# Kernel optimization log

Hardware: AMD Instinct MI355X
Metric: run time of the kernel (lower is better)

The kernel has to match this reference:

```python
import jax, jax.numpy as jnp
import numpy as np
from math import sqrt

B, LQ, LKV = 4, 1024, 1024
QD = KD = VD = 1024
MODEL_DIM = 1024
H = 16
HD = MODEL_DIM // H  # per-head model_dim = 64


def setup_inputs() -> dict:
    key = jax.random.key(0)
    ks = jax.random.split(key, 10)
    s = 0.02
    return {
        "queries": jax.random.normal(ks[0], (B, LQ, QD), jnp.float32),
        "context": jax.random.normal(ks[1], (B, LKV, KD), jnp.float32),
        # stacked per-head linear weights (torch Linear: y = x @ W.T + b); store as [H, in, out]
        "Wq": jax.random.normal(ks[2], (H, QD, HD), jnp.float32) * s,
        "bq": jax.random.normal(ks[3], (H, HD), jnp.float32) * s,
        "Wk": jax.random.normal(ks[4], (KD, HD * 1 * H), jnp.float32).reshape(H, KD, HD) * s,
        "bk": jax.random.normal(ks[5], (H, HD), jnp.float32) * s,
        "Wv": jax.random.normal(ks[6], (H, VD, HD), jnp.float32) * s,
        "bv": jax.random.normal(ks[7], (H, HD), jnp.float32) * s,
        "Wo": jax.random.normal(ks[8], (H * HD, MODEL_DIM), jnp.float32) * s,
        "bo": jax.random.normal(ks[9], (MODEL_DIM,), jnp.float32) * s,
    }


def reference(queries, context, Wq, bq, Wk, bk, Wv, bv, Wo, bo):
    # queries: [B,Lq,Dq]; context: [B,Lkv,Dk]
    # Per-head projections, batched over heads (equivalent to the torch per-head loop).
    q = jnp.einsum("bld,hdm->bhlm", queries, Wq) + bq[None, :, None, :]  # [B,H,Lq,hd]
    k = jnp.einsum("bld,hdm->bhlm", context, Wk) + bk[None, :, None, :]  # [B,H,Lkv,hd]
    v = jnp.einsum("bld,hdm->bhlm", context, Wv) + bv[None, :, None, :]  # [B,H,Lkv,hd]

    scale = 1.0 / sqrt(HD)
    scores = jnp.einsum("bhqd,bhkd->bhqk", q, k) * scale  # [B,H,Lq,Lkv]
    att = jax.nn.softmax(scores, axis=-1)
    head_out = jnp.einsum("bhqk,bhkd->bhqd", att, v)  # [B,H,Lq,hd]

    # torch concatenates heads along the last dim in head order 0..H-1
    multi = head_out.transpose(0, 2, 1, 3).reshape(B, LQ, H * HD)
    residual = q.transpose(0, 2, 1, 3).reshape(B, LQ, H * HD)

    out = multi @ Wo + bo  # [B,Lq,model_dim]
    return out, residual
```

## Files before the change

kernel.cpp:

```cpp
#include <hip/hip_runtime.h>
#include <hip/hip_bf16.h>


typedef unsigned short u16;
typedef __attribute__((ext_vector_type(8))) short short8;
typedef __attribute__((ext_vector_type(4))) float f32x4;

__device__ __forceinline__ float bf2f(u16 u) {
    union { unsigned int i; float f; } c;
    c.i = ((unsigned int)u) << 16;
    return c.f;
}

__device__ __forceinline__ u16 f2bf(float f) {
    unsigned int x = __float_as_uint(f);
    unsigned int r = (x + 0x7fffu + ((x >> 16) & 1u)) >> 16;
    return (u16)r;
}

__device__ __forceinline__ void glds16(u16* lds, const u16* g) {
    __builtin_amdgcn_global_load_lds(
        (const __attribute__((address_space(1))) void*)g,
        (__attribute__((address_space(3))) void*)lds, 16, 0, 0);
}

#define FENCE() asm volatile("" ::: "memory")
#define BAR() do { FENCE(); __builtin_amdgcn_s_barrier(); FENCE(); } while (0)
#define WAIT_LGKM0() do { asm volatile("s_waitcnt lgkmcnt(0)" ::: "memory"); \
                          __builtin_amdgcn_sched_barrier(0); } while (0)
#define WAIT_VM6() do { asm volatile("s_waitcnt vmcnt(6)" ::: "memory"); \
                        __builtin_amdgcn_sched_barrier(0); } while (0)
#define WAIT_VM4() do { asm volatile("s_waitcnt vmcnt(4)" ::: "memory"); \
                        __builtin_amdgcn_sched_barrier(0); } while (0)
#define WAIT_VM0() do { asm volatile("s_waitcnt vmcnt(0)" ::: "memory"); \
                        __builtin_amdgcn_sched_barrier(0); } while (0)

__global__ __launch_bounds__(256) void prep(
    const float* __restrict__ q, const float* __restrict__ ctx,
    const float* __restrict__ Wq, const float* __restrict__ Wk,
    const float* __restrict__ Wv, const float* __restrict__ Wo,
    u16* __restrict__ Aq, u16* __restrict__ Ac,
    u16* __restrict__ Wqt, u16* __restrict__ Wkt,
    u16* __restrict__ Wvt, u16* __restrict__ Wot)
{
    __shared__ float ls[64][65];
    const int t = threadIdx.x;
    int bid = blockIdx.x;

    if (bid < 4096) {
        const float* in = (bid < 2048) ? q : ctx;
        u16* out = (bid < 2048) ? Aq : Ac;
        size_t i = ((size_t)(bid & 2047) * 256 + t) * 8;
        float4 v0 = *(const float4*)(in + i);
        float4 v1 = *(const float4*)(in + i + 4);
        short8 p;
        p[0] = (short)f2bf(v0.x); p[1] = (short)f2bf(v0.y);
        p[2] = (short)f2bf(v0.z); p[3] = (short)f2bf(v0.w);
        p[4] = (short)f2bf(v1.x); p[5] = (short)f2bf(v1.y);
        p[6] = (short)f2bf(v1.z); p[7] = (short)f2bf(v1.w);
        *(short8*)(out + i) = p;
        return;
    }
    bid -= 4096;
    const float* in; u16* out; int C; size_t moff; int rt, ct;
    if (bid < 768) {
        const int m = bid >> 8, idx = bid & 255;
        in = (m == 0) ? Wq : (m == 1) ? Wk : Wv;
        out = (m == 0) ? Wqt : (m == 1) ? Wkt : Wvt;
        C = 64; rt = (idx & 15) * 64; ct = 0; moff = (size_t)(idx >> 4) * 65536;
    } else {
        const int idx = bid - 768;
        in = Wo; out = Wot; C = 1024; moff = 0;
        rt = (idx & 15) * 64; ct = (idx >> 4) * 64;
    }
    #pragma unroll
    for (int i = 0; i < 4; ++i) {
        int s = i * 256 + t;
        int row = s >> 4, chunk = s & 15;
        float4 v = *(const float4*)(in + moff + (size_t)(rt + row) * C + ct + chunk * 4);
        ls[row][chunk * 4 + 0] = v.x;
        ls[row][chunk * 4 + 1] = v.y;
        ls[row][chunk * 4 + 2] = v.z;
        ls[row][chunk * 4 + 3] = v.w;
    }
    __syncthreads();
    #pragma unroll
    for (int i = 0; i < 2; ++i) {
        int s = i * 256 + t;
        int n = s >> 3, kc = s & 7;
        short8 p;
        #pragma unroll
        for (int j = 0; j < 8; ++j) p[j] = (short)f2bf(ls[kc * 8 + j][n]);
        *(short8*)(out + moff + (size_t)(ct + n) * 1024 + rt + kc * 8) = p;
    }
}

__global__ __launch_bounds__(512) void gemm_qkv8(
    const u16* __restrict__ Aq, const u16* __restrict__ Ac,
    const u16* __restrict__ Wqt, const u16* __restrict__ Wkt,
    const u16* __restrict__ Wvt,
    const float* __restrict__ bq, const float* __restrict__ bk,
    const float* __restrict__ bv,
    u16* __restrict__ qws, u16* __restrict__ kws, u16* __restrict__ vtws)
{
    __shared__ u16 lds[2][2][256 * 64];

    const int tid = threadIdx.x;
    const int w = tid >> 6, lane = tid & 63;
    const int wr = w >> 2, wc = w & 3;
    const int quad = lane >> 4, c = lane & 15, cx = c & 7;
    const int sr = tid >> 3;
    const int gch = (tid & 7) ^ (sr & 7);

    const int f = blockIdx.x;
    const int xcd = f & 7, r = f >> 3;
    const int z = r >> 3;
    const int mt = xcd * 2 + ((r >> 2) & 1);
    const int nt = r & 3;
    const int m0 = mt * 256, n0 = nt * 256;

    const u16* A = (z == 0) ? Aq : Ac;
    const u16* Wt = (z == 0) ? Wqt : (z == 1) ? Wkt : Wvt;
    const float* bias = (z == 0) ? bq : (z == 1) ? bk : bv;

    const u16* gAt = A + (size_t)(m0 + sr) * 1024 + gch * 8;
    const u16* gBt = Wt + (size_t)(n0 + sr) * 1024 + gch * 8;

    auto stageA = [&](int par, int half, int t) {
        const u16* g = gAt + (size_t)half * 128 * 1024 + t * 64;
        u16* l = &lds[par][0][(half * 128 + w * 8) * 64];
        glds16(l, g);
        glds16(l + 64 * 64, g + (size_t)64 * 1024);
    };
    auto stageB = [&](int par, int half, int t) {
        const u16* g = gBt + (size_t)half * 128 * 1024 + t * 64;
        u16* l = &lds[par][1][(half * 128 + w * 8) * 64];
        glds16(l, g);
        glds16(l + 64 * 64, g + (size_t)64 * 1024);
    };

    f32x4 acc[8][4] = {};
    short8 aq[4][2], bA[2][2], bB[2][2];

    auto ldA = [&](int par, int mh) {
        #pragma unroll
        for (int mf = 0; mf < 4; ++mf)
            #pragma unroll
            for (int ks = 0; ks < 2; ++ks)
                aq[mf][ks] = *(const short8*)&lds[par][0][
                    (wr * 128 + mh * 64 + mf * 16 + c) * 64 + (((ks * 4 + quad) ^ cx) * 8)];
    };
    auto ldB = [&](int par, int nh, short8 (&bq_)[2][2]) {
        #pragma unroll
        for (int nf = 0; nf < 2; ++nf)
            #pragma unroll
            for (int ks = 0; ks < 2; ++ks)
                bq_[nf][ks] = *(const short8*)&lds[par][1][
                    (wc * 64 + nh * 32 + nf * 16 + c) * 64 + (((ks * 4 + quad) ^ cx) * 8)];
    };
    auto mma = [&](int mh, int nh, short8 (&bq_)[2][2]) {
        #pragma unroll
        for (int mf = 0; mf < 4; ++mf)
            #pragma unroll
            for (int nf = 0; nf < 2; ++nf)
                #pragma unroll
                for (int ks = 0; ks < 2; ++ks)
                    acc[mh * 4 + mf][nh * 2 + nf] =
                        __builtin_amdgcn_mfma_f32_16x16x32_bf16(
                            aq[mf][ks], bq_[nf][ks], acc[mh * 4 + mf][nh * 2 + nf], 0, 0, 0);
    };

    stageB(0, 0, 0); stageB(0, 1, 0); stageA(0, 0, 0); stageA(0, 1, 0);
    stageB(1, 0, 1); stageB(1, 1, 1);
    WAIT_VM4(); BAR();

    #pragma unroll 1
    for (int i = 0; i < 8; ++i) {
        const int o = 2 * i + 1, e = 2 * i + 2;

        ldA(0, 0); ldB(0, 0, bA);
        stageA(1, 0, o);
        BAR(); WAIT_LGKM0();
        __builtin_amdgcn_s_setprio(1); mma(0, 0, bA); __builtin_amdgcn_s_setprio(0);
        BAR();
        ldB(0, 1, bB);
        stageA(1, 1, o);
        BAR(); WAIT_LGKM0();
        __builtin_amdgcn_s_setprio(1); mma(0, 1, bB); __builtin_amdgcn_s_setprio(0);
        BAR();
        ldA(0, 1);
        if (i < 7) stageB(0, 0, e);
        BAR(); WAIT_LGKM0();
        __builtin_amdgcn_s_setprio(1); mma(1, 1, bB); __builtin_amdgcn_s_setprio(0);
        BAR();
        if (i < 7) stageB(0, 1, e);
        BAR();
        __builtin_amdgcn_s_setprio(1); mma(1, 0, bA); __builtin_amdgcn_s_setprio(0);
        if (i < 7) { WAIT_VM4(); } else { WAIT_VM0(); }
        BAR();
        ldA(1, 0); ldB(1, 0, bA);
        if (i < 7) stageA(0, 0, e);
        BAR(); WAIT_LGKM0();
        __builtin_amdgcn_s_setprio(1); mma(0, 0, bA); __builtin_amdgcn_s_setprio(0);
        BAR();
        ldB(1, 1, bB);
        if (i < 7) stageA(0, 1, e);
        BAR(); WAIT_LGKM0();
        __builtin_amdgcn_s_setprio(1); mma(0, 1, bB); __builtin_amdgcn_s_setprio(0);
        BAR();
        ldA(1, 1);
        if (i < 7) stageB(1, 0, e + 1);
        BAR(); WAIT_LGKM0();
        __builtin_amdgcn_s_setprio(1); mma(1, 1, bB); __builtin_amdgcn_s_setprio(0);
        BAR();
        if (i < 7) stageB(1, 1, e + 1);
        BAR();
        __builtin_amdgcn_s_setprio(1); mma(1, 0, bA); __builtin_amdgcn_s_setprio(0);
        if (i < 7) WAIT_VM4();
        BAR();
    }

    const int h = nt * 4 + wc;
    const int b = m0 >> 10;
    const int lbase = (m0 & 1023) + wr * 128;

    float bb[4];
    #pragma unroll
    for (int cn = 0; cn < 4; ++cn)
        bb[cn] = bias[h * 64 + (cn >> 1) * 32 + (cn & 1) * 16 + c];

    if (z < 2) {
        u16* dst = (z == 0) ? qws : kws;
        const float scale = (z == 0) ? 0.125f : 1.0f;
        u16* dbase = dst + (size_t)(b * 16 + h) * 1024 * 64;
        #pragma unroll
        for (int mi = 0; mi < 8; ++mi) {
            const int ro = (mi >> 2) * 64 + (mi & 3) * 16;
            const int rowb = lbase + ro + quad * 4;
            #pragma unroll
            for (int rr = 0; rr < 4; ++rr) {
                u16* drow = dbase + (size_t)(rowb + rr) * 64;
                #pragma unroll
                for (int cn = 0; cn < 4; ++cn) {
                    const int hd = (cn >> 1) * 32 + (cn & 1) * 16 + c;
                    drow[hd] = f2bf((acc[mi][cn][rr] + bb[cn]) * scale);
                }
            }
        }
    } else {
        u16* dbase = vtws + (size_t)(b * 16 + h) * 64 * 1024;
        #pragma unroll
        for (int mi = 0; mi < 8; ++mi) {
            const int ro = (mi >> 2) * 64 + (mi & 3) * 16;
            const int l0 = lbase + ro + quad * 4;
            #pragma unroll
            for (int cn = 0; cn < 4; ++cn) {
                const int hd = (cn >> 1) * 32 + (cn & 1) * 16 + c;
                ushort4 pk;
                pk.x = f2bf(acc[mi][cn][0] + bb[cn]);
                pk.y = f2bf(acc[mi][cn][1] + bb[cn]);
                pk.z = f2bf(acc[mi][cn][2] + bb[cn]);
                pk.w = f2bf(acc[mi][cn][3] + bb[cn]);
                *(ushort4*)(dbase + (size_t)hd * 1024 + l0) = pk;
            }
        }
    }
}

__global__ __launch_bounds__(256) void gemm_out(
    const u16* __restrict__ A, const u16* __restrict__ Wot,
    const float* __restrict__ bo, float* __restrict__ out)
{
    __shared__ u16 As[2][128 * 64];
    __shared__ u16 Bs[2][64 * 64];
    const int f = blockIdx.x;
    const int xcd = f & 7, k = f >> 3;
    const int m0 = (xcd * 4 + (k & 3)) * 128;
    const int n0 = (k >> 2) * 64;
    const int t = threadIdx.x;
    const int w = t >> 6, lane = t & 63;
    const int quad = lane >> 4, c = lane & 15;
    const int cx = c & 7;

    const int sr = w * 8 + (lane >> 3);
    const int gch = (lane & 7) ^ ((lane >> 3) & 7);
    const u16* gA = A + (size_t)(m0 + sr) * 1024 + gch * 8;
    const u16* gB = Wot + (size_t)(n0 + sr) * 1024 + gch * 8;

    const int arow = (w >> 1) * 64 + c;
    const int brow = (w & 1) * 32 + c;

    auto stage = [&](int par, int kt) {
        #pragma unroll
        for (int i = 0; i < 4; ++i)
            glds16(As[par] + (i * 32 + w * 8) * 64, gA + (size_t)i * 32 * 1024 + kt);
        #pragma unroll
        for (int i = 0; i < 2; ++i)
            glds16(Bs[par] + (i * 32 + w * 8) * 64, gB + (size_t)i * 32 * 1024 + kt);
    };

    f32x4 acc[4][2] = {};
    stage(0, 0);
    stage(1, 64);
    #pragma unroll 1
    for (int i = 0; i < 16; ++i) {
        const int cur = i & 1;
        if (i < 15) { WAIT_VM6(); } else { WAIT_VM0(); }
        BAR();
        #pragma unroll
        for (int kh = 0; kh < 2; ++kh) {
            const int ch = (kh * 4 + quad);
            short8 af[4], bf[2];
            #pragma unroll
            for (int rs = 0; rs < 4; ++rs)
                af[rs] = *(const short8*)(As[cur] + (arow + rs * 16) * 64 + (ch ^ cx) * 8);
            #pragma unroll
            for (int cs = 0; cs < 2; ++cs)
                bf[cs] = *(const short8*)(Bs[cur] + (brow + cs * 16) * 64 + (ch ^ cx) * 8);
            #pragma unroll
            for (int rs = 0; rs < 4; ++rs)
                #pragma unroll
                for (int cs = 0; cs < 2; ++cs)
                    acc[rs][cs] = __builtin_amdgcn_mfma_f32_16x16x32_bf16(
                        af[rs], bf[cs], acc[rs][cs], 0, 0, 0);
        }
        BAR();
        if (i < 14) stage(cur, (i + 2) * 64);
    }

    const int nb = n0 + (w & 1) * 32;
    float bb[2];
    #pragma unroll
    for (int cs = 0; cs < 2; ++cs) bb[cs] = bo[nb + cs * 16 + c];

    #pragma unroll
    for (int rs = 0; rs < 4; ++rs) {
        #pragma unroll
        for (int r = 0; r < 4; ++r) {
            const int row = m0 + (w >> 1) * 64 + rs * 16 + quad * 4 + r;
            float* orow = out + (size_t)row * 1024 + nb;
            #pragma unroll
            for (int cs = 0; cs < 2; ++cs)
                orow[cs * 16 + c] = acc[rs][cs][r] + bb[cs];
        }
    }
}

__global__ __launch_bounds__(256) void attn_mfma(
    const u16* __restrict__ qws, const u16* __restrict__ kws,
    const u16* __restrict__ vtws, u16* __restrict__ multi,
    float* __restrict__ resid)
{
    __shared__ u16 Ks[2][64 * 64];
    __shared__ u16 Vs[2][64 * 64];
    __shared__ u16 Ps[4][16 * 64];
    const int t = threadIdx.x;
    const int wave = t >> 6, lane = t & 63;
    const int quad = lane >> 4, c = lane & 15;
    const int cx = c & 7;
    const int f = blockIdx.x;
    const int xcd = f & 7, j = f >> 3;
    const int bh = xcd * 8 + (j & 7);
    const int qt = j >> 3;
    const int b = bh >> 4, h = bh & 15;
    const int q0 = qt * 128 + wave * 32;

    const u16* qb = qws + ((size_t)bh * 1024 + q0) * 64;
    const u16* kb = kws + (size_t)bh * 65536;
    const u16* vb = vtws + (size_t)bh * 65536;

    short8 qa[2][2];
    #pragma unroll
    for (int rb = 0; rb < 2; ++rb) {
        qa[rb][0] = *(const short8*)(qb + (size_t)(rb * 16 + c) * 64 + quad * 8);
        qa[rb][1] = *(const short8*)(qb + (size_t)(rb * 16 + c) * 64 + 32 + quad * 8);
    }

    const int srow = wave * 16 + (lane >> 3);
    const int gch = (lane & 7) ^ ((lane >> 3) & 7);
    const u16* gK0 = kb + (size_t)srow * 64 + gch * 8;
    const u16* gK1 = kb + (size_t)(srow + 8) * 64 + gch * 8;
    const u16* gV0 = vb + (size_t)srow * 1024 + gch * 8;
    const u16* gV1 = vb + (size_t)(srow + 8) * 1024 + gch * 8;

    auto stage = [&](int par, int kt) {
        glds16(Ks[par] + (wave * 16) * 64,     gK0 + (size_t)kt * 64);
        glds16(Ks[par] + (wave * 16 + 8) * 64, gK1 + (size_t)kt * 64);
        glds16(Vs[par] + (wave * 16) * 64,     gV0 + kt);
        glds16(Vs[par] + (wave * 16 + 8) * 64, gV1 + kt);
    };

    f32x4 O[2][4] = {};
    float ps[2][4] = {};
    u16* pw = &Ps[wave][0];

    stage(0, 0);
    stage(1, 64);

    #pragma unroll 1
    for (int i = 0; i < 16; ++i) {
        const int cur = i & 1;
        if (i < 15) { WAIT_VM4(); } else { WAIT_VM0(); }
        BAR();

        const u16* Kc = Ks[cur];
        const u16* Vc = Vs[cur];

        short8 kf[4][2], vf[4][2];
        #pragma unroll
        for (int nt = 0; nt < 4; ++nt) {
            const u16* kr = Kc + (nt * 16 + c) * 64;
            kf[nt][0] = *(const short8*)(kr + ((quad ^ cx)) * 8);
            kf[nt][1] = *(const short8*)(kr + (((4 + quad) ^ cx)) * 8);
            const u16* vr = Vc + (nt * 16 + c) * 64;
            vf[nt][0] = *(const short8*)(vr + ((quad ^ cx)) * 8);
            vf[nt][1] = *(const short8*)(vr + (((4 + quad) ^ cx)) * 8);
        }

        #pragma unroll
        for (int rb = 0; rb < 2; ++rb) {
            f32x4 s[4];
            __builtin_amdgcn_s_setprio(1);
            #pragma unroll
            for (int nt = 0; nt < 4; ++nt) {
                f32x4 z = {};
                z = __builtin_amdgcn_mfma_f32_16x16x32_bf16(qa[rb][0], kf[nt][0], z, 0, 0, 0);
                z = __builtin_amdgcn_mfma_f32_16x16x32_bf16(qa[rb][1], kf[nt][1], z, 0, 0, 0);
                s[nt] = z;
            }
            __builtin_amdgcn_s_setprio(0);

            #pragma unroll
            for (int nt = 0; nt < 4; ++nt)
                #pragma unroll
                for (int r = 0; r < 4; ++r) {
                    float p = __expf(s[nt][r]);
                    ps[rb][r] += p;
                    const int prow = quad * 4 + r;
                    pw[prow * 64 + (((nt * 2 + (c >> 3)) ^ (prow & 7)) * 8) + (c & 7)]
                        = (u16)(__float_as_uint(p) >> 16);
                }
            short8 pa0 = *(const short8*)(pw + c * 64 + ((quad ^ cx)) * 8);
            short8 pa1 = *(const short8*)(pw + c * 64 + (((4 + quad) ^ cx)) * 8);

            __builtin_amdgcn_s_setprio(1);
            #pragma unroll
            for (int nt = 0; nt < 4; ++nt) {
                O[rb][nt] = __builtin_amdgcn_mfma_f32_16x16x32_bf16(pa0, vf[nt][0], O[rb][nt], 0, 0, 0);
                O[rb][nt] = __builtin_amdgcn_mfma_f32_16x16x32_bf16(pa1, vf[nt][1], O[rb][nt], 0, 0, 0);
            }
            __builtin_amdgcn_s_setprio(0);
        }

        BAR();
        if (i < 14) stage(cur, (i + 2) * 64);
    }

    #pragma unroll
    for (int rb = 0; rb < 2; ++rb) {
        float inv[4];
        #pragma unroll
        for (int r = 0; r < 4; ++r) {
            float sum = ps[rb][r];
            sum += __shfl_xor(sum, 1);
            sum += __shfl_xor(sum, 2);
            sum += __shfl_xor(sum, 4);
            sum += __shfl_xor(sum, 8);
            inv[r] = 1.0f / sum;
        }
        u16* ob = multi + ((size_t)b * 1024 + q0 + rb * 16 + quad * 4) * 1024 + h * 64 + c;
        #pragma unroll
        for (int r = 0; r < 4; ++r) {
            u16* orow = ob + (size_t)r * 1024;
            orow[0]  = f2bf(O[rb][0][r] * inv[r]);
            orow[16] = f2bf(O[rb][1][r] * inv[r]);
            orow[32] = f2bf(O[rb][2][r] * inv[r]);
            orow[48] = f2bf(O[rb][3][r] * inv[r]);
        }

        float* rr = resid + ((size_t)b * 1024 + q0 + rb * 16 + c) * 1024 + h * 64;
        #pragma unroll
        for (int jj = 0; jj < 8; ++jj) {
            rr[quad * 8 + jj]      = bf2f((u16)qa[rb][0][jj]) * 8.0f;
            rr[32 + quad * 8 + jj] = bf2f((u16)qa[rb][1][jj]) * 8.0f;
        }
    }
}

extern "C" void kernel_launch(void* const* d_in, const int* in_sizes, int n_in,
                              void* d_out, int out_size, void* d_ws, size_t ws_size,
                              hipStream_t stream) {
    const float* queries = (const float*)d_in[0];
    const float* context = (const float*)d_in[1];
    const float* Wq = (const float*)d_in[2];
    const float* bq = (const float*)d_in[3];
    const float* Wk = (const float*)d_in[4];
    const float* bk = (const float*)d_in[5];
    const float* Wv = (const float*)d_in[6];
    const float* bv = (const float*)d_in[7];
    const float* Wo = (const float*)d_in[8];
    const float* bo = (const float*)d_in[9];

    float* out = (float*)d_out;
    float* resid = out + (size_t)4 * 1024 * 1024;

    const size_t M1 = 1024 * 1024;
    u16* Aq   = (u16*)d_ws;
    u16* Ac   = Aq + 4 * M1;
    u16* Wqt  = Ac + 4 * M1;
    u16* Wkt  = Wqt + M1;
    u16* Wvt  = Wkt + M1;
    u16* Wot  = Wvt + M1;
    u16* qws  = Wot + M1;
    u16* kws  = qws + 4 * M1;
    u16* vtws = kws + 4 * M1;
    u16* mws  = vtws + 4 * M1;

    prep<<<5120, 256, 0, stream>>>(queries, context, Wq, Wk, Wv, Wo,
                                   Aq, Ac, Wqt, Wkt, Wvt, Wot);
    gemm_qkv8<<<192, 512, 0, stream>>>(Aq, Ac, Wqt, Wkt, Wvt,
                                       bq, bk, bv, qws, kws, vtws);
    attn_mfma<<<512, 256, 0, stream>>>(qws, kws, vtws, mws, resid);
    gemm_out<<<512, 256, 0, stream>>>(mws, Wot, bo, out);
}
```

Baseline: 190.8 us.

## Replace 8-phase interleaved QKV GEMM schedule with simple double-buffered loop

The QKV projection GEMM drops its hand-interleaved 8-phase schedule, which split tile staging across many barriers and used setprio around MFMA groups. It now uses a plain double-buffered loop: wait for the current tile, run all four MFMA quadrants, then issue the global-to-LDS load for the tile two steps ahead. This cuts barrier count and scheduling complexity, but gives up the fine-grained overlap of LDS reads and global loads with MFMA work and removes the explicit priority hints.

```diff
diff --git a/kernel.cpp b/kernel.cpp
--- a/kernel.cpp
+++ b/kernel.cpp
@@ -26,8 +26,8 @@
 
 #define FENCE() asm volatile("" ::: "memory")
 #define BAR() do { FENCE(); __builtin_amdgcn_s_barrier(); FENCE(); } while (0)
-#define WAIT_LGKM0() do { asm volatile("s_waitcnt lgkmcnt(0)" ::: "memory"); \
-                          __builtin_amdgcn_sched_barrier(0); } while (0)
+#define WAIT_VM8() do { asm volatile("s_waitcnt vmcnt(8)" ::: "memory"); \
+                        __builtin_amdgcn_sched_barrier(0); } while (0)
 #define WAIT_VM6() do { asm volatile("s_waitcnt vmcnt(6)" ::: "memory"); \
                         __builtin_amdgcn_sched_barrier(0); } while (0)
 #define WAIT_VM4() do { asm volatile("s_waitcnt vmcnt(4)" ::: "memory"); \
@@ -95,7 +95,7 @@
     }
 }
 
-__global__ __launch_bounds__(512) void gemm_qkv8(
+__global__ __launch_bounds__(512) void gemm_qkv2(
     const u16* __restrict__ Aq, const u16* __restrict__ Ac,
     const u16* __restrict__ Wqt, const u16* __restrict__ Wkt,
     const u16* __restrict__ Wvt,
@@ -126,17 +126,14 @@
     const u16* gAt = A + (size_t)(m0 + sr) * 1024 + gch * 8;
     const u16* gBt = Wt + (size_t)(n0 + sr) * 1024 + gch * 8;
 
-    auto stageA = [&](int par, int half, int t) {
-        const u16* g = gAt + (size_t)half * 128 * 1024 + t * 64;
-        u16* l = &lds[par][0][(half * 128 + w * 8) * 64];
-        glds16(l, g);
-        glds16(l + 64 * 64, g + (size_t)64 * 1024);
-    };
-    auto stageB = [&](int par, int half, int t) {
-        const u16* g = gBt + (size_t)half * 128 * 1024 + t * 64;
-        u16* l = &lds[par][1][(half * 128 + w * 8) * 64];
-        glds16(l, g);
-        glds16(l + 64 * 64, g + (size_t)64 * 1024);
+    auto stage = [&](int par, int t) {
+        #pragma unroll
+        for (int i = 0; i < 4; ++i) {
+            glds16(&lds[par][0][(i * 64 + w * 8) * 64],
+                   gAt + (size_t)(i * 64) * 1024 + t * 64);
+            glds16(&lds[par][1][(i * 64 + w * 8) * 64],
+                   gBt + (size_t)(i * 64) * 1024 + t * 64);
+        }
     };
 
     f32x4 acc[8][4] = {};
@@ -170,54 +167,23 @@
                             aq[mf][ks], bq_[nf][ks], acc[mh * 4 + mf][nh * 2 + nf], 0, 0, 0);
     };
 
-    stageB(0, 0, 0); stageB(0, 1, 0); stageA(0, 0, 0); stageA(0, 1, 0);
-    stageB(1, 0, 1); stageB(1, 1, 1);
-    WAIT_VM4(); BAR();
-
+    stage(0, 0);
+    stage(1, 1);
     #pragma unroll 1
-    for (int i = 0; i < 8; ++i) {
-        const int o = 2 * i + 1, e = 2 * i + 2;
-
-        ldA(0, 0); ldB(0, 0, bA);
-        stageA(1, 0, o);
-        BAR(); WAIT_LGKM0();
-        __builtin_amdgcn_s_setprio(1); mma(0, 0, bA); __builtin_amdgcn_s_setprio(0);
-        BAR();
-        ldB(0, 1, bB);
-        stageA(1, 1, o);
-        BAR(); WAIT_LGKM0();
-        __builtin_amdgcn_s_setprio(1); mma(0, 1, bB); __builtin_amdgcn_s_setprio(0);
-        BAR();
-        ldA(0, 1);
-        if (i < 7) stageB(0, 0, e);
-        BAR(); WAIT_LGKM0();
-        __builtin_amdgcn_s_setprio(1); mma(1, 1, bB); __builtin_amdgcn_s_setprio(0);
-        BAR();
-        if (i < 7) stageB(0, 1, e);
-        BAR();
-        __builtin_amdgcn_s_setprio(1); mma(1, 0, bA); __builtin_amdgcn_s_setprio(0);
-        if (i < 7) { WAIT_VM4(); } else { WAIT_VM0(); }
-        BAR();
-        ldA(1, 0); ldB(1, 0, bA);
-        if (i < 7) stageA(0, 0, e);
-        BAR(); WAIT_LGKM0();
-        __builtin_amdgcn_s_setprio(1); mma(0, 0, bA); __builtin_amdgcn_s_setprio(0);
-        BAR();
-        ldB(1, 1, bB);
-        if (i < 7) stageA(0, 1, e);
-        BAR(); WAIT_LGKM0();
-        __builtin_amdgcn_s_setprio(1); mma(0, 1, bB); __builtin_amdgcn_s_setprio(0);
-        BAR();
-        ldA(1, 1);
-        if (i < 7) stageB(1, 0, e + 1);
-        BAR(); WAIT_LGKM0();
-        __builtin_amdgcn_s_setprio(1); mma(1, 1, bB); __builtin_amdgcn_s_setprio(0);
-        BAR();
-        if (i < 7) stageB(1, 1, e + 1);
-        BAR();
-        __builtin_amdgcn_s_setprio(1); mma(1, 0, bA); __builtin_amdgcn_s_setprio(0);
-        if (i < 7) WAIT_VM4();
-        BAR();
+    for (int i = 0; i < 16; ++i) {
+        const int cur = i & 1;
+        if (i < 15) { WAIT_VM8(); } else { WAIT_VM0(); }
+        BAR();
+        ldA(cur, 0);
+        ldB(cur, 0, bA);
+        mma(0, 0, bA);
+        ldB(cur, 1, bB);
+        mma(0, 1, bB);
+        ldA(cur, 1);
+        mma(1, 1, bB);
+        mma(1, 0, bA);
+        BAR();
+        if (i < 14) stage(cur, i + 2);
     }
 
     const int h = nt * 4 + wc;
@@ -518,7 +484,7 @@
 
     prep<<<5120, 256, 0, stream>>>(queries, context, Wq, Wk, Wv, Wo,
                                    Aq, Ac, Wqt, Wkt, Wvt, Wot);
-    gemm_qkv8<<<192, 512, 0, stream>>>(Aq, Ac, Wqt, Wkt, Wvt,
+    gemm_qkv2<<<192, 512, 0, stream>>>(Aq, Ac, Wqt, Wkt, Wvt,
                                        bq, bk, bv, qws, kws, vtws);
     attn_mfma<<<512, 256, 0, stream>>>(qws, kws, vtws, mws, resid);
     gemm_out<<<512, 256, 0, stream>>>(mws, Wot, bo, out);
```

Result: no change. 188.4 us (-1.2%).
